# Performance work log

Hardware: AMD Instinct MI355X
Metric: run time of the kernel (lower is better)

Reference implementation:

```python
import jax, jax.numpy as jnp
import numpy as np

DIMS, K_SIZE, V_SIZE, SEQ_LEN = 1024, 128, 128, 2048
MINUS = -100.0


def setup_inputs() -> dict:
    key = jax.random.key(0)
    k1, k2, k3, k4, k5 = jax.random.split(key, 5)
    B, S = 8, 2048
    minibatch = jax.random.normal(k1, (B, S, DIMS), dtype=jnp.float32)
    # Linear params (torch nn.Linear default init scale ~ U(-1/sqrt(fan_in), ...)); use scaled normals
    s = 1.0 / np.sqrt(DIMS)
    Wk = jax.random.normal(k2, (DIMS, K_SIZE), dtype=jnp.float32) * s
    bk = jax.random.normal(k3, (K_SIZE,), dtype=jnp.float32) * s
    Wv = jax.random.normal(k4, (DIMS, V_SIZE), dtype=jnp.float32) * s
    bv = jax.random.normal(k5, (V_SIZE,), dtype=jnp.float32) * s
    return {"minibatch": minibatch, "Wk": Wk, "bk": bk, "Wv": Wv, "bv": bv,
            "current_seq_len": S}


def reference(minibatch, Wk, bk, Wv, bv, current_seq_len):
    # keys == queries (shared projection, as in the original forward)
    keys = minibatch @ Wk + bk              # [B,S,K]
    values = minibatch @ Wv + bv            # [B,S,V]
    S = current_seq_len
    mask = jnp.tril(jnp.ones((S, S), dtype=jnp.float32))  # [S,S] lower-triangular
    scores = jnp.einsum('bsk,btk->bst', keys, keys) / np.sqrt(K_SIZE)
    logits = mask * scores + MINUS * (1.0 - mask)
    probs = jax.nn.softmax(logits, axis=2)
    read = jnp.einsum('bst,btv->bsv', probs, values)  # [B,S,V]
    return jnp.concatenate([minibatch, read], axis=2)  # [B,S,dims+V]
```

## Files before the change

kernel.cpp:

```cpp
#include <hip/hip_runtime.h>
#include <hip/hip_bf16.h>

#define BATCH 8
#define SEQ   2048
#define DMS   1024
#define KSZ   128
#define OD    1152

typedef unsigned short u16;
typedef unsigned int   u32;
typedef __attribute__((ext_vector_type(4)))  float  f32x4;
typedef __attribute__((ext_vector_type(16))) float  f32x16;
typedef __attribute__((ext_vector_type(8)))  __bf16 bf16x8;

union U128 { uint4 u4; bf16x8 b8; u16 us[8]; u32 u[4]; };

__device__ inline u16 f2bf(float f) {
  union { __bf16 h; u16 u; } c;
  c.h = (__bf16)f;
  return c.u;
}

__device__ inline float fexp2(float x) {
  float r;
  asm("v_exp_f32 %0, %1" : "=v"(r) : "v"(x));
  return r;
}

__device__ inline f32x4 mfma16(bf16x8 a, bf16x8 b, f32x4 c) {
  return __builtin_amdgcn_mfma_f32_16x16x32_bf16(a, b, c, 0, 0, 0);
}
__device__ inline f32x16 mfma32(bf16x8 a, bf16x8 b, f32x16 c) {
  return __builtin_amdgcn_mfma_f32_32x32x16_bf16(a, b, c, 0, 0, 0);
}

__device__ inline uint4 pack8bf(float4 a, float4 b) {
  U128 w;
  w.us[0] = f2bf(a.x); w.us[1] = f2bf(a.y);
  w.us[2] = f2bf(a.z); w.us[3] = f2bf(a.w);
  w.us[4] = f2bf(b.x); w.us[5] = f2bf(b.y);
  w.us[6] = f2bf(b.z); w.us[7] = f2bf(b.w);
  return w.u4;
}

__device__ inline void glds16(const u16* src, u16* ldsDst) {
  __builtin_amdgcn_global_load_lds(
      (const __attribute__((address_space(1))) u32*)src,
      (__attribute__((address_space(3))) u32*)ldsDst, 16, 0, 0);
}

#define BSTRIDE 262144

__global__ void __launch_bounds__(256) prep_kernel(
    const float* __restrict__ Wk, const float* __restrict__ Wv,
    u16* __restrict__ Wslabs)
{
  int T = blockIdx.x * 256 + threadIdx.x;
  int n  = T & 255;
  int kc = (T >> 8) * 8;
  int s  = kc >> 7;
  int kk = kc & 127;
  const float* src = (n < 128) ? (Wk + n) : (Wv + (n - 128));
  U128 w;
#pragma unroll
  for (int j = 0; j < 8; ++j) w.us[j] = f2bf(src[(size_t)(kc + j) * KSZ]);
  u16* dst = Wslabs + s * 32768 + n * 128 + (kk ^ ((n & 7) << 3));
  *(uint4*)dst = w.u4;
}

__global__ void __launch_bounds__(256, 1) gemm_kernel(
    const float* __restrict__ X, const u16* __restrict__ Wslabs,
    const float* __restrict__ bk, const float* __restrict__ bv,
    u16* __restrict__ Kfrag, u16* __restrict__ Vfrag)
{
  __shared__ u16 Ws[256 * 128];

  const int tid  = threadIdx.x;
  const int lane = tid & 63;
  const int wv   = tid >> 6;
  const int l15  = lane & 15;
  const int g    = lane >> 4;
  const int m0   = blockIdx.x * 64;

  const float* xrow = X + (size_t)(m0 + wv * 16 + l15) * DMS + g * 8;

  f32x4 acc[16];
#pragma unroll
  for (int nf = 0; nf < 16; ++nf) acc[nf] = (f32x4){0.f, 0.f, 0.f, 0.f};

#pragma unroll 1
  for (int s = 0; s < 8; ++s) {
    __syncthreads();
    {
      const u16* ws = Wslabs + s * 32768 + tid * 8;
      u16* wd = Ws + tid * 8;
#pragma unroll
      for (int c = 0; c < 16; ++c) glds16(ws + c * 2048, wd + c * 2048);
    }
    float4 xv[8];
#pragma unroll
    for (int ks = 0; ks < 4; ++ks) {
      xv[ks * 2]     = *(const float4*)(xrow + s * 128 + ks * 32);
      xv[ks * 2 + 1] = *(const float4*)(xrow + s * 128 + ks * 32 + 4);
    }
    __syncthreads();
#pragma unroll
    for (int ks = 0; ks < 4; ++ks) {
      U128 aw; aw.u4 = pack8bf(xv[ks * 2], xv[ks * 2 + 1]);
#pragma unroll
      for (int nf = 0; nf < 16; ++nf) {
        int n = nf * 16 + l15;
        int idx = n * 128 + ((ks * 32 + g * 8) ^ ((n & 7) << 3));
        U128 u; u.u4 = *(const uint4*)(Ws + idx);
        acc[nf] = mfma16(aw.b8, u.b8, acc[nf]);
      }
    }
  }

  __syncthreads();
#pragma unroll
  for (int nf = 0; nf < 16; ++nf) {
    int n = nf * 16 + l15;
    float bs = (n < 128) ? bk[n] : bv[n - 128];
#pragma unroll
    for (int j = 0; j < 4; ++j) {
      int srow = wv * 16 + g * 4 + j;
      Ws[srow * 256 + (n ^ ((srow & 7) << 3))] = f2bf(acc[nf][j] + bs);
    }
  }
  __syncthreads();

  const int bb   = m0 >> 11;
  const int tloc = (m0 & 2047) >> 5;

  {
    int sl  = tid >> 2;
    int t2  = tloc + (sl >> 5);
    int l31 = sl & 31;
#pragma unroll
    for (int h = 0; h < 2; ++h) {
      int ks2 = (tid & 3) * 2 + h;
      u16* dst = Kfrag + (size_t)bb * BSTRIDE + (size_t)(t2 * 8 + ks2) * 512 + l31 * 8;
#pragma unroll
      for (int hi2 = 0; hi2 < 2; ++hi2) {
        int n = ks2 * 16 + hi2 * 8;
        uint4 v = *(const uint4*)&Ws[sl * 256 + (n ^ ((sl & 7) << 3))];
        *(uint4*)(dst + hi2 * 256) = v;
      }
    }
  }
  {
    int l31 = tid & 31;
    int vb2 = (tid >> 5) & 3;
    int th  = (tid >> 7) & 1;
    int n   = 128 + vb2 * 32 + l31;
#pragma unroll
    for (int p = 0; p < 2; ++p) {
      int t2 = tloc + p;
#pragma unroll
      for (int hi = 0; hi < 2; ++hi) {
        U128 wvv;
#pragma unroll
        for (int j = 0; j < 8; ++j) {
          int srow = p * 32 + th * 16 + hi * 8 + j;
          wvv.us[j] = Ws[srow * 256 + (n ^ ((srow & 7) << 3))];
        }
        u16* dst = Vfrag + (size_t)bb * BSTRIDE +
                   (size_t)((t2 * 4 + vb2) * 2 + th) * 512 + hi * 256 + l31 * 8;
        *(uint4*)dst = wvv.u4;
      }
    }
  }
}

__global__ void __launch_bounds__(256, 2) attn_kernel(
    const u16* __restrict__ Kfrag, const u16* __restrict__ Vfrag,
    const float* __restrict__ X, float* __restrict__ out)
{
  __shared__ float Om[4][128][33];
  __shared__ float Ml[4][2][32];
  __shared__ float Wm[4][32];
  __shared__ float Li[32];

  const int tid  = threadIdx.x;
  const int lane = tid & 63;
  const int w    = tid >> 6;
  const int l31  = lane & 31;
  const int hi   = lane >> 5;

  const int bi = blockIdx.x;
  const int b  = bi & 7;
  const int qt = (bi < 256) ? (63 - (bi >> 3)) : ((bi >> 3) - 32);
  const int q0 = qt * 32;

  const u16* Kb = Kfrag + (size_t)b * BSTRIDE;
  const u16* Vb = Vfrag + (size_t)b * BSTRIDE;
  const int loff = hi * 256 + l31 * 8;

  bf16x8 qf[8];
  {
    const u16* qp = Kb + (size_t)(qt * 8) * 512 + loff;
#pragma unroll
    for (int ks = 0; ks < 8; ++ks) {
      U128 u; u.u4 = *(const uint4*)(qp + ks * 512); qf[ks] = u.b8;
    }
  }

  f32x16 o[4];
#pragma unroll
  for (int vb2 = 0; vb2 < 4; ++vb2)
#pragma unroll
    for (int i = 0; i < 16; ++i) o[vb2][i] = 0.f;

  float mrun = -3.0e38f, lsum = 0.f;
  const float SC  = 0.08838834764831845f;
  const float L2E = 1.44269504088896341f;

  bf16x8 kf[8];
  {
    int ti0 = (w <= qt) ? w : 0;
    const u16* kp = Kb + (size_t)(ti0 * 8) * 512 + loff;
#pragma unroll
    for (int ks = 0; ks < 8; ++ks) {
      U128 u; u.u4 = *(const uint4*)(kp + ks * 512); kf[ks] = u.b8;
    }
  }

  for (int ti = w; ti <= qt; ti += 4) {
    bf16x8 vf[4][2];
    {
      const u16* vp = Vb + (size_t)(ti * 8) * 512 + loff;
#pragma unroll
      for (int vb2 = 0; vb2 < 4; ++vb2)
#pragma unroll
        for (int th = 0; th < 2; ++th) {
          U128 u; u.u4 = *(const uint4*)(vp + (vb2 * 2 + th) * 512);
          vf[vb2][th] = u.b8;
        }
    }
    f32x16 s;
#pragma unroll
    for (int i = 0; i < 16; ++i) s[i] = 0.f;
#pragma unroll
    for (int ks = 0; ks < 8; ++ks) s = mfma32(kf[ks], qf[ks], s);
    {
      int tin = (ti + 4 <= qt) ? ti + 4 : ti;
      const u16* kp = Kb + (size_t)(tin * 8) * 512 + loff;
#pragma unroll
      for (int ks = 0; ks < 8; ++ks) {
        U128 u; u.u4 = *(const uint4*)(kp + ks * 512); kf[ks] = u.b8;
      }
    }
    float sv[16];
#pragma unroll
    for (int r = 0; r < 16; ++r) sv[r] = s[r] * SC;
    if (ti == qt) {
#pragma unroll
      for (int r = 0; r < 16; ++r) {
        int toff = (r & 3) + 8 * (r >> 2) + 4 * hi;
        if (toff > l31) sv[r] = -3.0e38f;
      }
    }
    float mx = sv[0];
#pragma unroll
    for (int r = 1; r < 16; ++r) mx = fmaxf(mx, sv[r]);
    mx = fmaxf(mx, __shfl_xor(mx, 32));
    float p[16];
    float ps = 0.f;
    if (__all(mx - mrun <= 8.0f)) {
#pragma unroll
      for (int r = 0; r < 16; ++r) { p[r] = fexp2((sv[r] - mrun) * L2E); ps += p[r]; }
      ps += __shfl_xor(ps, 32);
      lsum += ps;
    } else {
      float mnew = fmaxf(mrun, mx);
      float al = fexp2((mrun - mnew) * L2E);
#pragma unroll
      for (int r = 0; r < 16; ++r) { p[r] = fexp2((sv[r] - mnew) * L2E); ps += p[r]; }
      ps += __shfl_xor(ps, 32);
      lsum = lsum * al + ps;
      mrun = mnew;
#pragma unroll
      for (int vb2 = 0; vb2 < 4; ++vb2)
#pragma unroll
        for (int i = 0; i < 16; ++i) o[vb2][i] *= al;
    }
    u32 c01 = (u32)f2bf(p[0])  | ((u32)f2bf(p[1])  << 16);
    u32 c23 = (u32)f2bf(p[2])  | ((u32)f2bf(p[3])  << 16);
    u32 c45 = (u32)f2bf(p[4])  | ((u32)f2bf(p[5])  << 16);
    u32 c67 = (u32)f2bf(p[6])  | ((u32)f2bf(p[7])  << 16);
    u32 c89 = (u32)f2bf(p[8])  | ((u32)f2bf(p[9])  << 16);
    u32 cAB = (u32)f2bf(p[10]) | ((u32)f2bf(p[11]) << 16);
    u32 cCD = (u32)f2bf(p[12]) | ((u32)f2bf(p[13]) << 16);
    u32 cEF = (u32)f2bf(p[14]) | ((u32)f2bf(p[15]) << 16);
    u32 d01 = __shfl_xor(c01, 32);
    u32 d23 = __shfl_xor(c23, 32);
    u32 d45 = __shfl_xor(c45, 32);
    u32 d67 = __shfl_xor(c67, 32);
    u32 d89 = __shfl_xor(c89, 32);
    u32 dAB = __shfl_xor(cAB, 32);
    u32 dCD = __shfl_xor(cCD, 32);
    u32 dEF = __shfl_xor(cEF, 32);
    U128 pf1, pf2;
    pf1.u[0] = hi ? d45 : c01;
    pf1.u[1] = hi ? d67 : c23;
    pf1.u[2] = hi ? c45 : d01;
    pf1.u[3] = hi ? c67 : d23;
    pf2.u[0] = hi ? dCD : c89;
    pf2.u[1] = hi ? dEF : cAB;
    pf2.u[2] = hi ? cCD : d89;
    pf2.u[3] = hi ? cEF : dAB;
#pragma unroll
    for (int vb2 = 0; vb2 < 4; ++vb2) {
      o[vb2] = mfma32(vf[vb2][0], pf1.b8, o[vb2]);
      o[vb2] = mfma32(vf[vb2][1], pf2.b8, o[vb2]);
    }
  }

#pragma unroll
  for (int vb2 = 0; vb2 < 4; ++vb2)
#pragma unroll
    for (int r = 0; r < 16; ++r) {
      int v = vb2 * 32 + (r & 3) + 8 * (r >> 2) + 4 * hi;
      Om[w][v][l31] = o[vb2][r];
    }
  if (lane < 32) {
    Ml[w][0][l31] = mrun;
    Ml[w][1][l31] = lsum;
  }
  __syncthreads();

  if (tid < 32) {
    float m0 = Ml[0][0][tid], m1 = Ml[1][0][tid];
    float m2 = Ml[2][0][tid], m3 = Ml[3][0][tid];
    float M  = fmaxf(fmaxf(m0, m1), fmaxf(m2, m3));
    float w0 = fexp2((m0 - M) * L2E), w1 = fexp2((m1 - M) * L2E);
    float w2 = fexp2((m2 - M) * L2E), w3 = fexp2((m3 - M) * L2E);
    float L  = Ml[0][1][tid] * w0 + Ml[1][1][tid] * w1 +
               Ml[2][1][tid] * w2 + Ml[3][1][tid] * w3;
    Wm[0][tid] = w0; Wm[1][tid] = w1; Wm[2][tid] = w2; Wm[3][tid] = w3;
    Li[tid] = 1.f / L;
  }
  __syncthreads();

  {
    const int q = tid >> 3;
    const int vbase = (tid & 7) * 16;
    float wq0 = Wm[0][q], wq1 = Wm[1][q], wq2 = Wm[2][q], wq3 = Wm[3][q];
    float li = Li[q];
    float* orow = out + (size_t)(b * SEQ + q0 + q) * OD + 1024 + vbase;
#pragma unroll
    for (int i = 0; i < 16; i += 4) {
      float4 res;
      res.x = (Om[0][vbase + i + 0][q] * wq0 + Om[1][vbase + i + 0][q] * wq1 +
               Om[2][vbase + i + 0][q] * wq2 + Om[3][vbase + i + 0][q] * wq3) * li;
      res.y = (Om[0][vbase + i + 1][q] * wq0 + Om[1][vbase + i + 1][q] * wq1 +
               Om[2][vbase + i + 1][q] * wq2 + Om[3][vbase + i + 1][q] * wq3) * li;
      res.z = (Om[0][vbase + i + 2][q] * wq0 + Om[1][vbase + i + 2][q] * wq1 +
               Om[2][vbase + i + 2][q] * wq2 + Om[3][vbase + i + 2][q] * wq3) * li;
      res.w = (Om[0][vbase + i + 3][q] * wq0 + Om[1][vbase + i + 3][q] * wq1 +
               Om[2][vbase + i + 3][q] * wq2 + Om[3][vbase + i + 3][q] * wq3) * li;
      *(float4*)(orow + i) = res;
    }
  }

  {
#pragma unroll
    for (int r0 = 0; r0 < 32; r0 += 8) {
      float4 t[8];
#pragma unroll
      for (int j = 0; j < 8; ++j)
        t[j] = *((const float4*)(X + (size_t)(b * SEQ + q0 + r0 + j) * DMS) + tid);
#pragma unroll
      for (int j = 0; j < 8; ++j)
        *((float4*)(out + (size_t)(b * SEQ + q0 + r0 + j) * OD) + tid) = t[j];
    }
  }
}

extern "C" void kernel_launch(void* const* d_in, const int* in_sizes, int n_in,
                              void* d_out, int out_size, void* d_ws, size_t ws_size,
                              hipStream_t stream)
{
  const float* X  = (const float*)d_in[0];
  const float* Wk = (const float*)d_in[1];
  const float* bk = (const float*)d_in[2];
  const float* Wv = (const float*)d_in[3];
  const float* bv = (const float*)d_in[4];
  float* out = (float*)d_out;

  u16* Kfrag  = (u16*)d_ws;
  u16* Vfrag  = Kfrag + (size_t)BATCH * BSTRIDE;
  u16* Wslabs = Vfrag + (size_t)BATCH * BSTRIDE;

  prep_kernel<<<dim3(128), dim3(256), 0, stream>>>(Wk, Wv, Wslabs);
  gemm_kernel<<<dim3(256), dim3(256), 0, stream>>>(X, Wslabs, bk, bv, Kfrag, Vfrag);
  attn_kernel<<<dim3(512), dim3(256), 0, stream>>>(Kfrag, Vfrag, X, out);
}
```

Before: 74.83 us.

## Stage full X tile in LDS and stream MFMA-ready weight fragments from global

The projection GEMM previously staged weight slabs in LDS and read X directly from global per wave. Now each block converts its 64x1024 X tile to bf16 once into swizzled LDS. Each wave owns 64 output columns and reads pre-laid-out weight fragments straight from global, double-buffered in registers. The prep kernel emits weights in MFMA fragment order and the epilogue splits K and V scatter between waves. This removes the per-slab barriers and LDS weight traffic. In exchange it needs 128KB of LDS and relies on cache for the repeated weight reads.

```diff
diff --git a/kernel.cpp b/kernel.cpp
--- a/kernel.cpp
+++ b/kernel.cpp
@@ -43,132 +43,187 @@
   return w.u4;
 }
 
-__device__ inline void glds16(const u16* src, u16* ldsDst) {
-  __builtin_amdgcn_global_load_lds(
-      (const __attribute__((address_space(1))) u32*)src,
-      (__attribute__((address_space(3))) u32*)ldsDst, 16, 0, 0);
-}
-
 #define BSTRIDE 262144
+
 
 __global__ void __launch_bounds__(256) prep_kernel(
     const float* __restrict__ Wk, const float* __restrict__ Wv,
-    u16* __restrict__ Wslabs)
+    u16* __restrict__ Wfrag)
 {
   int T = blockIdx.x * 256 + threadIdx.x;
-  int n  = T & 255;
-  int kc = (T >> 8) * 8;
-  int s  = kc >> 7;
-  int kk = kc & 127;
+  int lane = T & 63;
+  int nf   = (T >> 6) & 15;
+  int ks   = T >> 10;
+  int l15  = lane & 15;
+  int g    = lane >> 4;
+  int n    = nf * 16 + l15;
   const float* src = (n < 128) ? (Wk + n) : (Wv + (n - 128));
+  int k0 = ks * 32 + g * 8;
   U128 w;
 #pragma unroll
-  for (int j = 0; j < 8; ++j) w.us[j] = f2bf(src[(size_t)(kc + j) * KSZ]);
-  u16* dst = Wslabs + s * 32768 + n * 128 + (kk ^ ((n & 7) << 3));
-  *(uint4*)dst = w.u4;
+  for (int j = 0; j < 8; ++j) w.us[j] = f2bf(src[(size_t)(k0 + j) * KSZ]);
+  *(uint4*)(Wfrag + (size_t)T * 8) = w.u4;
 }
 
 __global__ void __launch_bounds__(256, 1) gemm_kernel(
-    const float* __restrict__ X, const u16* __restrict__ Wslabs,
+    const float* __restrict__ X, const u16* __restrict__ Wfrag,
     const float* __restrict__ bk, const float* __restrict__ bv,
     u16* __restrict__ Kfrag, u16* __restrict__ Vfrag)
 {
-  __shared__ u16 Ws[256 * 128];
+  __shared__ u16 Xl[64 * 1024];
 
   const int tid  = threadIdx.x;
   const int lane = tid & 63;
-  const int wv   = tid >> 6;
+  const int w    = tid >> 6;
   const int l15  = lane & 15;
   const int g    = lane >> 4;
   const int m0   = blockIdx.x * 64;
 
-  const float* xrow = X + (size_t)(m0 + wv * 16 + l15) * DMS + g * 8;
-
-  f32x4 acc[16];
-#pragma unroll
-  for (int nf = 0; nf < 16; ++nf) acc[nf] = (f32x4){0.f, 0.f, 0.f, 0.f};
-
-#pragma unroll 1
-  for (int s = 0; s < 8; ++s) {
-    __syncthreads();
+  {
+    const int u   = tid & 127;
+    const int ro  = tid >> 7;
+#pragma unroll
+    for (int h = 0; h < 4; ++h) {
+      float4 t0[8], t1[8];
+#pragma unroll
+      for (int p = 0; p < 8; ++p) {
+        int row = (h * 8 + p) * 2 + ro;
+        const float4* xp = (const float4*)(X + (size_t)(m0 + row) * DMS + u * 8);
+        t0[p] = xp[0]; t1[p] = xp[1];
+      }
+#pragma unroll
+      for (int p = 0; p < 8; ++p) {
+        int row = (h * 8 + p) * 2 + ro;
+        *(uint4*)(Xl + row * 1024 + ((u * 8) ^ ((row & 7) << 3))) =
+            pack8bf(t0[p], t1[p]);
+      }
+    }
+  }
+  __syncthreads();
+
+  f32x4 acc[4][4];
+#pragma unroll
+  for (int i = 0; i < 4; ++i)
+#pragma unroll
+    for (int j = 0; j < 4; ++j) acc[i][j] = (f32x4){0.f, 0.f, 0.f, 0.f};
+
+  const u16* wbase = Wfrag + (w * 4) * 512 + lane * 8;
+
+  bf16x8 wfA[4], wfB[4];
+#pragma unroll
+  for (int nf = 0; nf < 4; ++nf) {
+    U128 u; u.u4 = *(const uint4*)(wbase + nf * 512); wfA[nf] = u.b8;
+  }
+
+#pragma unroll
+  for (int k2 = 0; k2 < 16; ++k2) {
     {
-      const u16* ws = Wslabs + s * 32768 + tid * 8;
-      u16* wd = Ws + tid * 8;
-#pragma unroll
-      for (int c = 0; c < 16; ++c) glds16(ws + c * 2048, wd + c * 2048);
-    }
-    float4 xv[8];
-#pragma unroll
-    for (int ks = 0; ks < 4; ++ks) {
-      xv[ks * 2]     = *(const float4*)(xrow + s * 128 + ks * 32);
-      xv[ks * 2 + 1] = *(const float4*)(xrow + s * 128 + ks * 32 + 4);
-    }
-    __syncthreads();
-#pragma unroll
-    for (int ks = 0; ks < 4; ++ks) {
-      U128 aw; aw.u4 = pack8bf(xv[ks * 2], xv[ks * 2 + 1]);
-#pragma unroll
-      for (int nf = 0; nf < 16; ++nf) {
-        int n = nf * 16 + l15;
-        int idx = n * 128 + ((ks * 32 + g * 8) ^ ((n & 7) << 3));
-        U128 u; u.u4 = *(const uint4*)(Ws + idx);
-        acc[nf] = mfma16(aw.b8, u.b8, acc[nf]);
-      }
+      const int ksn = 2 * k2 + 1;
+#pragma unroll
+      for (int nf = 0; nf < 4; ++nf) {
+        U128 u; u.u4 = *(const uint4*)(wbase + (size_t)ksn * 8192 + nf * 512);
+        wfB[nf] = u.b8;
+      }
+      const int ks = 2 * k2;
+      bf16x8 af[4];
+#pragma unroll
+      for (int mf = 0; mf < 4; ++mf) {
+        int m = mf * 16 + l15;
+        U128 u; u.u4 = *(const uint4*)(Xl + m * 1024 +
+                                       ((ks * 32 + g * 8) ^ ((m & 7) << 3)));
+        af[mf] = u.b8;
+      }
+#pragma unroll
+      for (int mf = 0; mf < 4; ++mf)
+#pragma unroll
+        for (int nf = 0; nf < 4; ++nf)
+          acc[mf][nf] = mfma16(af[mf], wfA[nf], acc[mf][nf]);
+    }
+    {
+      const int ksn = (k2 < 15) ? 2 * k2 + 2 : 0;
+#pragma unroll
+      for (int nf = 0; nf < 4; ++nf) {
+        U128 u; u.u4 = *(const uint4*)(wbase + (size_t)ksn * 8192 + nf * 512);
+        wfA[nf] = u.b8;
+      }
+      const int ks = 2 * k2 + 1;
+      bf16x8 af[4];
+#pragma unroll
+      for (int mf = 0; mf < 4; ++mf) {
+        int m = mf * 16 + l15;
+        U128 u; u.u4 = *(const uint4*)(Xl + m * 1024 +
+                                       ((ks * 32 + g * 8) ^ ((m & 7) << 3)));
+        af[mf] = u.b8;
+      }
+#pragma unroll
+      for (int mf = 0; mf < 4; ++mf)
+#pragma unroll
+        for (int nf = 0; nf < 4; ++nf)
+          acc[mf][nf] = mfma16(af[mf], wfB[nf], acc[mf][nf]);
     }
   }
 
   __syncthreads();
-#pragma unroll
-  for (int nf = 0; nf < 16; ++nf) {
-    int n = nf * 16 + l15;
-    float bs = (n < 128) ? bk[n] : bv[n - 128];
-#pragma unroll
-    for (int j = 0; j < 4; ++j) {
-      int srow = wv * 16 + g * 4 + j;
-      Ws[srow * 256 + (n ^ ((srow & 7) << 3))] = f2bf(acc[nf][j] + bs);
-    }
-  }
-  __syncthreads();
+
+  u16* Cw = Xl + w * 4096;
+  {
+    float bias[4];
+#pragma unroll
+    for (int nf = 0; nf < 4; ++nf) {
+      int n = w * 64 + nf * 16 + l15;
+      bias[nf] = (n < 128) ? bk[n] : bv[n - 128];
+    }
+#pragma unroll
+    for (int nf = 0; nf < 4; ++nf)
+#pragma unroll
+      for (int mf = 0; mf < 4; ++mf)
+#pragma unroll
+        for (int j = 0; j < 4; ++j) {
+          int s = mf * 16 + g * 4 + j;
+          int c = nf * 16 + l15;
+          Cw[s * 64 + (c ^ ((s & 7) << 3))] = f2bf(acc[mf][nf][j] + bias[nf]);
+        }
+  }
 
   const int bb   = m0 >> 11;
   const int tloc = (m0 & 2047) >> 5;
 
-  {
-    int sl  = tid >> 2;
-    int t2  = tloc + (sl >> 5);
-    int l31 = sl & 31;
-#pragma unroll
-    for (int h = 0; h < 2; ++h) {
-      int ks2 = (tid & 3) * 2 + h;
+  if (w < 2) {
+    const int sl  = lane;
+    const int t2  = tloc + (sl >> 5);
+    const int l31 = sl & 31;
+#pragma unroll
+    for (int kc = 0; kc < 4; ++kc) {
+      int ks2 = w * 4 + kc;
       u16* dst = Kfrag + (size_t)bb * BSTRIDE + (size_t)(t2 * 8 + ks2) * 512 + l31 * 8;
 #pragma unroll
       for (int hi2 = 0; hi2 < 2; ++hi2) {
-        int n = ks2 * 16 + hi2 * 8;
-        uint4 v = *(const uint4*)&Ws[sl * 256 + (n ^ ((sl & 7) << 3))];
+        uint4 v = *(const uint4*)&Cw[sl * 64 + ((kc * 16 + hi2 * 8) ^ ((sl & 7) << 3))];
         *(uint4*)(dst + hi2 * 256) = v;
       }
     }
-  }
-  {
-    int l31 = tid & 31;
-    int vb2 = (tid >> 5) & 3;
-    int th  = (tid >> 7) & 1;
-    int n   = 128 + vb2 * 32 + l31;
+  } else {
+    const int l31v   = lane & 31;
+    const int vb2loc = lane >> 5;
+    const int vb2    = (w - 2) * 2 + vb2loc;
+    const int ccol   = vb2loc * 32 + l31v;
 #pragma unroll
     for (int p = 0; p < 2; ++p) {
       int t2 = tloc + p;
 #pragma unroll
-      for (int hi = 0; hi < 2; ++hi) {
-        U128 wvv;
-#pragma unroll
-        for (int j = 0; j < 8; ++j) {
-          int srow = p * 32 + th * 16 + hi * 8 + j;
-          wvv.us[j] = Ws[srow * 256 + (n ^ ((srow & 7) << 3))];
+      for (int th = 0; th < 2; ++th)
+#pragma unroll
+        for (int hi = 0; hi < 2; ++hi) {
+          U128 wv;
+#pragma unroll
+          for (int j = 0; j < 8; ++j) {
+            int s = p * 32 + th * 16 + hi * 8 + j;
+            wv.us[j] = Cw[s * 64 + (ccol ^ ((s & 7) << 3))];
+          }
+          u16* dst = Vfrag + (size_t)bb * BSTRIDE +
+                     (size_t)((t2 * 4 + vb2) * 2 + th) * 512 + hi * 256 + l31v * 8;
+          *(uint4*)dst = wv.u4;
         }
-        u16* dst = Vfrag + (size_t)bb * BSTRIDE +
-                   (size_t)((t2 * 4 + vb2) * 2 + th) * 512 + hi * 256 + l31 * 8;
-        *(uint4*)dst = wvv.u4;
-      }
     }
   }
 }
@@ -389,11 +444,11 @@
   const float* bv = (const float*)d_in[4];
   float* out = (float*)d_out;
 
-  u16* Kfrag  = (u16*)d_ws;
-  u16* Vfrag  = Kfrag + (size_t)BATCH * BSTRIDE;
-  u16* Wslabs = Vfrag + (size_t)BATCH * BSTRIDE;
-
-  prep_kernel<<<dim3(128), dim3(256), 0, stream>>>(Wk, Wv, Wslabs);
-  gemm_kernel<<<dim3(256), dim3(256), 0, stream>>>(X, Wslabs, bk, bv, Kfrag, Vfrag);
+  u16* Kfrag = (u16*)d_ws;
+  u16* Vfrag = Kfrag + (size_t)BATCH * BSTRIDE;
+  u16* Wfrag = Vfrag + (size_t)BATCH * BSTRIDE;
+
+  prep_kernel<<<dim3(128), dim3(256), 0, stream>>>(Wk, Wv, Wfrag);
+  gemm_kernel<<<dim3(256), dim3(256), 0, stream>>>(X, Wfrag, bk, bv, Kfrag, Vfrag);
   attn_kernel<<<dim3(512), dim3(256), 0, stream>>>(Kfrag, Vfrag, X, out);
 }
```

Result: faster. 67.85 us (-9.3%).
